# Kernel tuning notes

Hardware: AMD Instinct MI355X
Metric: run time of the kernel (lower is better)

## Reference

```python
import jax, jax.numpy as jnp
import numpy as np

EMB = 512
HEADS = 16
WH, WW = 8, 8
N = WH * WW
B = 2048
CPB_HID = 512
EPS = 1e-12


def _buffers():
    # continuous relative coords table, shape (1, 2*WH-1, 2*WW-1, 2)
    ch = np.arange(-(WH - 1), WH, dtype=np.float32)
    cw = np.arange(-(WW - 1), WW, dtype=np.float32)
    t = np.stack(np.meshgrid(ch, cw, indexing='ij')).transpose(1, 2, 0)[None].copy()
    t[..., 0] /= (WH - 1)
    t[..., 1] /= (WW - 1)
    t *= 8.0
    t = np.sign(t) * np.log2(np.abs(t) + 1.0) / np.log2(8.0)
    # relative position index, shape (N, N), values in [0, (2*WH-1)*(2*WW-1))
    coords = np.stack(np.meshgrid(np.arange(WH), np.arange(WW), indexing='ij'))
    cf = coords.reshape(2, -1)
    rel = (cf[:, :, None] - cf[:, None, :]).transpose(1, 2, 0).copy()
    rel[..., 0] += WH - 1
    rel[..., 1] += WW - 1
    rel[..., 0] *= 2 * WW - 1
    idx = rel.sum(-1)
    return jnp.asarray(t, jnp.float32), jnp.asarray(idx, jnp.int32)


def setup_inputs() -> dict:
    key = jax.random.key(0)
    ks = jax.random.split(key, 8)
    rel_table, rel_index = _buffers()
    s = 0.02
    return {
        'x': jax.random.normal(ks[0], (B, N, EMB), jnp.float32),
        'qkv_w': jax.random.normal(ks[1], (3 * EMB, EMB), jnp.float32) * s,
        'q_bias': jnp.zeros((EMB,), jnp.float32),
        'v_bias': jnp.zeros((EMB,), jnp.float32),
        'flex_attn': jnp.full((HEADS, 1, 1), np.log(10.0), jnp.float32),
        'cpb_w1': jax.random.normal(ks[2], (CPB_HID, 2), jnp.float32) * s,
        'cpb_b1': jnp.zeros((CPB_HID,), jnp.float32),
        'cpb_w2': jax.random.normal(ks[3], (HEADS, CPB_HID), jnp.float32) * s,
        'proj_w': jax.random.normal(ks[4], (EMB, EMB), jnp.float32) * s,
        'proj_b': jnp.zeros((EMB,), jnp.float32),
        'rel_table': rel_table,
        'rel_index': rel_index,
    }


def reference(x, qkv_w, q_bias, v_bias, flex_attn, cpb_w1, cpb_b1, cpb_w2,
              proj_w, proj_b, rel_table, rel_index):
    Bx, Nx, C = x.shape
    H = HEADS
    D = C // H
    # qkv with bias only on q and v (k bias is zero), as in the torch code
    qkv_bias = jnp.concatenate([q_bias, jnp.zeros_like(v_bias), v_bias])
    qkv = x @ qkv_w.T + qkv_bias                      # (B, N, 3C)
    qkv = qkv.reshape(Bx, Nx, 3, H, D).transpose(2, 0, 3, 1, 4)
    q, k, v = qkv[0], qkv[1], qkv[2]                  # each (B, H, N, D)
    # cosine attention: L2-normalize q and k
    qn = q / jnp.maximum(jnp.linalg.norm(q, axis=-1, keepdims=True), EPS)
    kn = k / jnp.maximum(jnp.linalg.norm(k, axis=-1, keepdims=True), EPS)
    attn = jnp.einsum('bhnd,bhmd->bhnm', qn, kn)      # (B, H, N, N)
    # learned per-head temperature, clamped at 1/0.01
    scale = jnp.exp(jnp.minimum(flex_attn, jnp.log(jnp.float32(100.0))))  # (H,1,1)
    attn = attn * scale[None]
    # continuous relative position bias via MLP + gather
    bias_tab = jax.nn.relu(rel_table @ cpb_w1.T + cpb_b1) @ cpb_w2.T      # (1, 2WH-1, 2WW-1, H)
    bias_tab = bias_tab.reshape(-1, H)
    bias = bias_tab[rel_index.reshape(-1)].reshape(Nx, Nx, H)
    bias = 16.0 * jax.nn.sigmoid(bias.transpose(2, 0, 1))                 # (H, N, N)
    attn = jax.nn.softmax(attn + bias[None], axis=-1)
    out = jnp.einsum('bhnm,bhmd->bhnd', attn, v)      # (B, H, N, D)
    out = out.transpose(0, 2, 1, 3).reshape(Bx, Nx, C)
    return out @ proj_w.T + proj_b
```

## Files before the change

### kernel.cpp

```cpp
#include <hip/hip_runtime.h>

using bf16x8 = __attribute__((ext_vector_type(8))) short;
using f32x4  = __attribute__((ext_vector_type(4))) float;

static constexpr int EMB = 512, HEADS = 16, NTOK = 64, BWIN = 2048;
static constexpr int MROWS = BWIN * NTOK;
static constexpr int QKVN  = 3 * EMB;

__device__ __forceinline__ float bf2f(unsigned int u) {
  union { unsigned int i; float f; } c; c.i = u << 16; return c.f;
}
__device__ __forceinline__ unsigned short f2bf(float x) {
  union { float f; unsigned int i; } c; c.f = x;
  return (unsigned short)((c.i + 0x7fffu + ((c.i >> 16) & 1u)) >> 16);
}
__device__ __forceinline__ void gload_lds16(const void* g, void* l) {
  __builtin_amdgcn_global_load_lds((const __attribute__((address_space(1))) void*)g,
                                   (__attribute__((address_space(3))) void*)l, 16, 0, 0);
}

#define BARRIER() __builtin_amdgcn_s_barrier()
#define LGKM0()  do { asm volatile("s_waitcnt lgkmcnt(0)" ::: "memory"); \
                      __builtin_amdgcn_sched_barrier(0); } while (0)
#define VMCNT2() do { asm volatile("s_waitcnt vmcnt(2)" ::: "memory"); \
                      __builtin_amdgcn_sched_barrier(0); } while (0)

__global__ __launch_bounds__(256) void xcast(const float* __restrict__ x,
                                             unsigned short* __restrict__ xb) {
  size_t i = ((size_t)blockIdx.x * 256 + threadIdx.x) * 8;
  float4 a = *(const float4*)(x + i);
  float4 b = *(const float4*)(x + i + 4);
  ushort4 lo = make_ushort4(f2bf(a.x), f2bf(a.y), f2bf(a.z), f2bf(a.w));
  ushort4 hi = make_ushort4(f2bf(b.x), f2bf(b.y), f2bf(b.z), f2bf(b.w));
  *(ushort4*)(xb + i) = lo;
  *(ushort4*)(xb + i + 4) = hi;
}

__global__ void prep_weights(const float* __restrict__ qkv_w, const float* __restrict__ proj_w,
                             const float* __restrict__ q_bias, const float* __restrict__ v_bias,
                             unsigned short* __restrict__ wq, unsigned short* __restrict__ wp,
                             float* __restrict__ qkv_bias) {
  int i = blockIdx.x * 256 + threadIdx.x;
  wq[i] = f2bf(qkv_w[i]);
  if (i < EMB * EMB) wp[i] = f2bf(proj_w[i]);
  if (i < EMB) {
    qkv_bias[i]           = q_bias[i];
    qkv_bias[EMB + i]     = 0.f;
    qkv_bias[2 * EMB + i] = v_bias[i];
  }
}

__global__ __launch_bounds__(64) void cpb_mlp(const float* __restrict__ tbl,
                        const float* __restrict__ w1, const float* __restrict__ b1,
                        const float* __restrict__ w2, float* __restrict__ tab) {
  __shared__ float hid[512];
  const int p = blockIdx.x, t = threadIdx.x;
  const float t0 = tbl[p * 2], t1 = tbl[p * 2 + 1];
  #pragma unroll
  for (int s = 0; s < 8; ++s) {
    int j = t + s * 64;
    hid[j] = fmaxf(0.f, t0 * w1[j * 2] + t1 * w1[j * 2 + 1] + b1[j]);
  }
  __syncthreads();
  const int h = t >> 2, q = t & 3;
  float sum = 0.f;
  for (int j = q * 128; j < q * 128 + 128; ++j) sum += hid[j] * w2[h * 512 + j];
  sum += __shfl_xor(sum, 1);
  sum += __shfl_xor(sum, 2);
  if (q == 0) tab[p * 16 + h] = sum;
}

__global__ void cpb_expand(const float* __restrict__ tab, const int* __restrict__ rel_index,
                           float* __restrict__ bias16) {
  int e = blockIdx.x * 256 + threadIdx.x;
  int h = e >> 12, ij = e & 4095;
  float x = tab[rel_index[ij] * 16 + h];
  bias16[e] = 16.f / (1.f + __expf(-x));
}

template<bool OUT_F32, int NBX, int KT>
__global__ __launch_bounds__(512, 2) void gemm256(const unsigned short* __restrict__ Ap,
    const unsigned short* __restrict__ Bp, const float* __restrict__ bias,
    void* __restrict__ Cp, int M, int N) {
  __shared__ unsigned short As[2][256 * 64];
  __shared__ unsigned short Bs[2][256 * 64];
  constexpr int NT = KT / 64;
  constexpr int NITER = NT / 2;
  const int t = threadIdx.x;
  const int l = t & 63, w = t >> 6;
  const int lr = l & 15, lg = l >> 4;
  const int q8 = gridDim.x >> 3;
  const int wgid = (blockIdx.x & 7) * q8 + (blockIdx.x >> 3);
  const int n0 = (wgid % NBX) * 256, m0 = (wgid / NBX) * 256;
  const int wm = (w >> 2) * 128, wn = (w & 3) * 64;
  const int ha128 = (w >> 2) * 128;
  const int srow = t >> 3;
  const int scol = ((t & 7) ^ (srow & 7)) << 3;
  const unsigned short* Abase = Ap + (size_t)m0 * KT;
  const unsigned short* Bbase = Bp + (size_t)n0 * KT;

  f32x4 acc[8][4];
  #pragma unroll
  for (int i = 0; i < 8; ++i)
    #pragma unroll
    for (int j = 0; j < 4; ++j) acc[i][j] = (f32x4){0.f, 0.f, 0.f, 0.f};
  bf16x8 afr[4][2], bfr[4][2];

  auto stage_half = [&](int d, int kt, int half, bool isA) {
    const unsigned short* g = (isA ? Abase : Bbase)
        + (size_t)(half * 128 + srow) * KT + kt * 64 + scol;
    unsigned short* lds = (isA ? &As[d][0] : &Bs[d][0]) + half * 8192 + (t >> 6) * 512;
    gload_lds16(g, lds);
    gload_lds16(g + (size_t)64 * KT, lds + 4096);
  };
  auto ldA4 = [&](int d, int mb) {
    #pragma unroll
    for (int m = 0; m < 4; ++m) {
      int row = ha128 + (mb + m) * 16 + lr;
      #pragma unroll
      for (int ks = 0; ks < 2; ++ks)
        afr[m][ks] = *(const bf16x8*)(&As[d][row * 64 + ((((ks << 2) + lg) ^ (lr & 7)) << 3)]);
    }
  };
  auto ldB2 = [&](int d, int nb) {
    #pragma unroll
    for (int n = 0; n < 2; ++n) {
      int row = wn + (nb + n) * 16 + lr;
      #pragma unroll
      for (int ks = 0; ks < 2; ++ks)
        bfr[nb + n][ks] = *(const bf16x8*)(&Bs[d][row * 64 + ((((ks << 2) + lg) ^ (lr & 7)) << 3)]);
    }
  };
  auto mfmaQ = [&](int mb, int nb) {
    __builtin_amdgcn_s_setprio(1);
    #pragma unroll
    for (int ks = 0; ks < 2; ++ks)
      #pragma unroll
      for (int m = 0; m < 4; ++m)
        #pragma unroll
        for (int n = 0; n < 2; ++n)
          acc[mb + m][nb + n] = __builtin_amdgcn_mfma_f32_16x16x32_bf16(
              afr[m][ks], bfr[nb + n][ks], acc[mb + m][nb + n], 0, 0, 0);
    __builtin_amdgcn_s_setprio(0);
  };

  stage_half(0, 0, 0, true);  stage_half(0, 0, 1, true);
  stage_half(0, 0, 0, false); stage_half(0, 0, 1, false);
  stage_half(1, (NT > 1 ? 1 : 0), 0, true);
  VMCNT2();
  BARRIER();

  for (int i = 0; i < NITER; ++i) {
    const int kt1 = 2 * i + 1;
    const int kt2 = (2 * i + 2 < NT) ? 2 * i + 2 : NT - 1;
    const int kt3 = (2 * i + 3 < NT) ? 2 * i + 3 : NT - 1;
    ldA4(0, 0); ldB2(0, 0);
    stage_half(1, kt1, 1, true);
    BARRIER(); LGKM0(); mfmaQ(0, 0); BARRIER();
    ldB2(0, 2);
    stage_half(1, kt1, 0, false);
    BARRIER(); LGKM0(); mfmaQ(0, 2); BARRIER();
    ldA4(0, 4);
    stage_half(1, kt1, 1, false);
    BARRIER(); LGKM0(); mfmaQ(4, 2); BARRIER();
    stage_half(0, kt2, 0, true);
    VMCNT2(); BARRIER(); mfmaQ(4, 0); BARRIER();
    ldA4(1, 0); ldB2(1, 0);
    stage_half(0, kt2, 1, true);
    BARRIER(); LGKM0(); mfmaQ(0, 0); BARRIER();
    ldB2(1, 2);
    stage_half(0, kt2, 0, false);
    BARRIER(); LGKM0(); mfmaQ(0, 2); BARRIER();
    ldA4(1, 4);
    stage_half(0, kt2, 1, false);
    BARRIER(); LGKM0(); mfmaQ(4, 2); BARRIER();
    stage_half(1, kt3, 0, true);
    VMCNT2(); BARRIER(); mfmaQ(4, 0); BARRIER();
  }

  #pragma unroll
  for (int mf = 0; mf < 8; ++mf)
    #pragma unroll
    for (int nf = 0; nf < 4; ++nf)
      #pragma unroll
      for (int r = 0; r < 4; ++r) {
        int mm = m0 + wm + mf * 16 + lg * 4 + r;
        int nn = n0 + wn + nf * 16 + lr;
        float v = acc[mf][nf][r] + bias[nn];
        if (OUT_F32) ((float*)Cp)[(size_t)mm * N + nn] = v;
        else ((unsigned short*)Cp)[(size_t)mm * N + nn] = f2bf(v);
      }
}

__device__ __forceinline__ bf16x8 load_norm_frag(const unsigned short* p, float s) {
  uint4 raw = *(const uint4*)p;
  float f[8];
  f[0] = bf2f(raw.x & 0xffffu); f[1] = bf2f(raw.x >> 16);
  f[2] = bf2f(raw.y & 0xffffu); f[3] = bf2f(raw.y >> 16);
  f[4] = bf2f(raw.z & 0xffffu); f[5] = bf2f(raw.z >> 16);
  f[6] = bf2f(raw.w & 0xffffu); f[7] = bf2f(raw.w >> 16);
  float ss = 0.f;
  #pragma unroll
  for (int j = 0; j < 8; ++j) ss += f[j] * f[j];
  ss += __shfl_xor(ss, 16);
  ss += __shfl_xor(ss, 32);
  float inv = s / fmaxf(sqrtf(ss), 1e-12f);
  bf16x8 v;
  #pragma unroll
  for (int j = 0; j < 8; ++j) v[j] = (short)f2bf(f[j] * inv);
  return v;
}

__global__ __launch_bounds__(64, 2) void attn_win(const unsigned short* __restrict__ qkv,
    const float* __restrict__ bias16, const float* __restrict__ flex,
    unsigned short* __restrict__ aout) {
  __shared__ __align__(16) char smem[16640];
  float* S           = (float*)smem;
  unsigned short* P  = (unsigned short*)smem;
  unsigned short* vT = (unsigned short*)(smem + 9216);
  const int l = threadIdx.x;
  const int lr = l & 15, lg = l >> 4;
  const int g = (blockIdx.x & 7) * (gridDim.x >> 3) + (blockIdx.x >> 3);
  const int b = g >> 4;
  const int h = g & 15;
  const unsigned short* base = qkv + (size_t)b * NTOK * QKVN;
  const float scale = __expf(fminf(flex[h], 4.6051701860f));

  const uint4* vp = (const uint4*)(base + (size_t)l * QKVN + 2 * EMB + h * 32);
  uint4 v0 = vp[0], v1 = vp[1], v2 = vp[2], v3 = vp[3];

  bf16x8 aq[4], bk[4];
  #pragma unroll
  for (int i = 0; i < 4; ++i)
    aq[i] = load_norm_frag(base + (size_t)(i * 16 + lr) * QKVN + h * 32 + lg * 8, scale);
  #pragma unroll
  for (int i = 0; i < 4; ++i)
    bk[i] = load_norm_frag(base + (size_t)(i * 16 + lr) * QKVN + EMB + h * 32 + lg * 8, 1.f);

  const f32x4 z = (f32x4){0.f, 0.f, 0.f, 0.f};
  f32x4 sacc[4][4];
  #pragma unroll
  for (int i = 0; i < 4; ++i)
    #pragma unroll
    for (int j = 0; j < 4; ++j)
      sacc[i][j] = __builtin_amdgcn_mfma_f32_16x16x32_bf16(aq[i], bk[j], z, 0, 0, 0);

  const float* bh = bias16 + (size_t)h * 4096;
  #pragma unroll
  for (int i = 0; i < 4; ++i)
    #pragma unroll
    for (int j = 0; j < 4; ++j)
      #pragma unroll
      for (int r = 0; r < 4; ++r) {
        int row = i * 16 + lg * 4 + r, col = j * 16 + lr;
        S[row * 65 + col] = sacc[i][j][r] + bh[row * 64 + col];
      }

  float rowv[64];
  float mx = -1e30f;
  #pragma unroll
  for (int j = 0; j < 64; ++j) { rowv[j] = S[l * 65 + j]; mx = fmaxf(mx, rowv[j]); }
  asm volatile("" ::: "memory");
  float sum = 0.f;
  #pragma unroll
  for (int s = 0; s < 8; ++s) {
    bf16x8 pk;
    #pragma unroll
    for (int m = 0; m < 8; ++m) {
      float e = __expf(rowv[s * 8 + m] - mx);
      sum += e;
      pk[m] = (short)f2bf(e);
    }
    *(bf16x8*)(P + l * 72 + s * 8) = pk;
  }
  const float inv = 1.f / sum;

  {
    unsigned int wd[16] = {v0.x, v0.y, v0.z, v0.w, v1.x, v1.y, v1.z, v1.w,
                           v2.x, v2.y, v2.z, v2.w, v3.x, v3.y, v3.z, v3.w};
    #pragma unroll
    for (int d = 0; d < 32; ++d) {
      unsigned short val = (d & 1) ? (unsigned short)(wd[d >> 1] >> 16)
                                   : (unsigned short)(wd[d >> 1] & 0xffffu);
      vT[d * 72 + l] = val;
    }
  }
  asm volatile("" ::: "memory");

  f32x4 oacc[4][2];
  #pragma unroll
  for (int i = 0; i < 4; ++i) { oacc[i][0] = z; oacc[i][1] = z; }
  #pragma unroll
  for (int ks = 0; ks < 2; ++ks) {
    bf16x8 ap[4], bv[2];
    #pragma unroll
    for (int i = 0; i < 4; ++i)
      ap[i] = *(const bf16x8*)(P + (i * 16 + lr) * 72 + ks * 32 + lg * 8);
    #pragma unroll
    for (int jd = 0; jd < 2; ++jd)
      bv[jd] = *(const bf16x8*)(vT + (jd * 16 + lr) * 72 + ks * 32 + lg * 8);
    #pragma unroll
    for (int i = 0; i < 4; ++i)
      #pragma unroll
      for (int jd = 0; jd < 2; ++jd)
        oacc[i][jd] = __builtin_amdgcn_mfma_f32_16x16x32_bf16(ap[i], bv[jd], oacc[i][jd], 0, 0, 0);
  }
  #pragma unroll
  for (int i = 0; i < 4; ++i)
    #pragma unroll
    for (int jd = 0; jd < 2; ++jd)
      #pragma unroll
      for (int r = 0; r < 4; ++r) {
        int tok = i * 16 + lg * 4 + r, d = jd * 16 + lr;
        float val = oacc[i][jd][r] * __shfl(inv, tok);
        aout[(size_t)(b * NTOK + tok) * EMB + h * 32 + d] = f2bf(val);
      }
}

extern "C" void kernel_launch(void* const* d_in, const int* in_sizes, int n_in,
                              void* d_out, int out_size, void* d_ws, size_t ws_size,
                              hipStream_t stream) {
  const float* x         = (const float*)d_in[0];
  const float* qkv_w     = (const float*)d_in[1];
  const float* q_bias    = (const float*)d_in[2];
  const float* v_bias    = (const float*)d_in[3];
  const float* flex      = (const float*)d_in[4];
  const float* cpb_w1    = (const float*)d_in[5];
  const float* cpb_b1    = (const float*)d_in[6];
  const float* cpb_w2    = (const float*)d_in[7];
  const float* proj_w    = (const float*)d_in[8];
  const float* proj_b    = (const float*)d_in[9];
  const float* rel_table = (const float*)d_in[10];
  const int*   rel_index = (const int*)d_in[11];

  char* ws = (char*)d_ws;
  unsigned short* qkv_bf = (unsigned short*)(ws + 0);
  unsigned short* xb     = (unsigned short*)(ws + 402653184ull);
  unsigned short* ao_bf  = (unsigned short*)(ws + 402653184ull);
  unsigned short* wq_bf  = (unsigned short*)(ws + 536870912ull);
  unsigned short* wp_bf  = (unsigned short*)(ws + 538443776ull);
  float* qkv_bias        = (float*)(ws + 538968064ull);
  float* tab             = (float*)(ws + 538974208ull);
  float* bias16          = (float*)(ws + 538988608ull);

  xcast<<<32768, 256, 0, stream>>>(x, xb);
  prep_weights<<<3072, 256, 0, stream>>>(qkv_w, proj_w, q_bias, v_bias, wq_bf, wp_bf, qkv_bias);
  cpb_mlp<<<225, 64, 0, stream>>>(rel_table, cpb_w1, cpb_b1, cpb_w2, tab);
  cpb_expand<<<256, 256, 0, stream>>>(tab, rel_index, bias16);
  gemm256<false, 6, EMB><<<3072, 512, 0, stream>>>(
      xb, wq_bf, qkv_bias, (void*)qkv_bf, MROWS, QKVN);
  attn_win<<<BWIN * HEADS, 64, 0, stream>>>(qkv_bf, bias16, flex, ao_bf);
  gemm256<true, 2, EMB><<<1024, 512, 0, stream>>>(
      ao_bf, wp_bf, proj_b, d_out, MROWS, EMB);
}
```

Before: 644.7 us.

## Shrink GEMM tile to 128x256 with K-step 32 and four blocks per CU

Replaces the 256x256 GEMM tile with a 128x256 tile and a 32-wide K step. The LDS footprint shrinks and a new XOR swizzle is used, which allows four blocks per CU instead of two. The pipeline schedule is reworked to fewer stages per iteration and the grid size doubles. This trades less data reuse per tile and more global traffic for higher occupancy and latency hiding; each wave now holds fewer accumulators.

```diff
diff --git a/kernel.cpp b/kernel.cpp
--- a/kernel.cpp
+++ b/kernel.cpp
@@ -22,7 +22,7 @@
 #define BARRIER() __builtin_amdgcn_s_barrier()
 #define LGKM0()  do { asm volatile("s_waitcnt lgkmcnt(0)" ::: "memory"); \
                       __builtin_amdgcn_sched_barrier(0); } while (0)
-#define VMCNT2() do { asm volatile("s_waitcnt vmcnt(2)" ::: "memory"); \
+#define VMCNT1() do { asm volatile("s_waitcnt vmcnt(1)" ::: "memory"); \
                       __builtin_amdgcn_sched_barrier(0); } while (0)
 
 __global__ __launch_bounds__(256) void xcast(const float* __restrict__ x,
@@ -79,107 +79,90 @@
 }
 
 template<bool OUT_F32, int NBX, int KT>
-__global__ __launch_bounds__(512, 2) void gemm256(const unsigned short* __restrict__ Ap,
+__global__ __launch_bounds__(512, 4) void gemm128(const unsigned short* __restrict__ Ap,
     const unsigned short* __restrict__ Bp, const float* __restrict__ bias,
     void* __restrict__ Cp, int M, int N) {
-  __shared__ unsigned short As[2][256 * 64];
-  __shared__ unsigned short Bs[2][256 * 64];
-  constexpr int NT = KT / 64;
+  __shared__ unsigned short As[2][128 * 32];
+  __shared__ unsigned short Bs[2][256 * 32];
+  constexpr int NT = KT / 32;
   constexpr int NITER = NT / 2;
   const int t = threadIdx.x;
   const int l = t & 63, w = t >> 6;
   const int lr = l & 15, lg = l >> 4;
   const int q8 = gridDim.x >> 3;
   const int wgid = (blockIdx.x & 7) * q8 + (blockIdx.x >> 3);
-  const int n0 = (wgid % NBX) * 256, m0 = (wgid / NBX) * 256;
-  const int wm = (w >> 2) * 128, wn = (w & 3) * 64;
-  const int ha128 = (w >> 2) * 128;
-  const int srow = t >> 3;
-  const int scol = ((t & 7) ^ (srow & 7)) << 3;
+  const int n0 = (wgid % NBX) * 256, m0 = (wgid / NBX) * 128;
+  const int wm = (w >> 2) * 64, wn = (w & 3) * 64;
+  const int srow = t >> 2;
+  const int sphys = t & 3;
   const unsigned short* Abase = Ap + (size_t)m0 * KT;
   const unsigned short* Bbase = Bp + (size_t)n0 * KT;
 
-  f32x4 acc[8][4];
-  #pragma unroll
-  for (int i = 0; i < 8; ++i)
+  f32x4 acc[4][4];
+  #pragma unroll
+  for (int i = 0; i < 4; ++i)
     #pragma unroll
     for (int j = 0; j < 4; ++j) acc[i][j] = (f32x4){0.f, 0.f, 0.f, 0.f};
-  bf16x8 afr[4][2], bfr[4][2];
-
-  auto stage_half = [&](int d, int kt, int half, bool isA) {
-    const unsigned short* g = (isA ? Abase : Bbase)
-        + (size_t)(half * 128 + srow) * KT + kt * 64 + scol;
-    unsigned short* lds = (isA ? &As[d][0] : &Bs[d][0]) + half * 8192 + (t >> 6) * 512;
-    gload_lds16(g, lds);
-    gload_lds16(g + (size_t)64 * KT, lds + 4096);
-  };
-  auto ldA4 = [&](int d, int mb) {
+  bf16x8 afr[4], bfr[4];
+
+  auto stageA = [&](int d, int kt) {
+    int logc = (sphys ^ ((srow >> 1) & 3)) << 3;
+    gload_lds16(Abase + (size_t)srow * KT + kt * 32 + logc, &As[d][w * 512]);
+  };
+  auto stageB = [&](int d, int kt, int pass) {
+    int row = pass * 128 + srow;
+    int logc = (sphys ^ ((row >> 1) & 3)) << 3;
+    gload_lds16(Bbase + (size_t)row * KT + kt * 32 + logc,
+                &Bs[d][pass * 4096 + w * 512]);
+  };
+  auto ldA4 = [&](int d) {
     #pragma unroll
     for (int m = 0; m < 4; ++m) {
-      int row = ha128 + (mb + m) * 16 + lr;
-      #pragma unroll
-      for (int ks = 0; ks < 2; ++ks)
-        afr[m][ks] = *(const bf16x8*)(&As[d][row * 64 + ((((ks << 2) + lg) ^ (lr & 7)) << 3)]);
+      int row = wm + m * 16 + lr;
+      afr[m] = *(const bf16x8*)(&As[d][row * 32 + ((lg ^ ((row >> 1) & 3)) << 3)]);
     }
   };
-  auto ldB2 = [&](int d, int nb) {
-    #pragma unroll
-    for (int n = 0; n < 2; ++n) {
-      int row = wn + (nb + n) * 16 + lr;
-      #pragma unroll
-      for (int ks = 0; ks < 2; ++ks)
-        bfr[nb + n][ks] = *(const bf16x8*)(&Bs[d][row * 64 + ((((ks << 2) + lg) ^ (lr & 7)) << 3)]);
+  auto ldB4 = [&](int d) {
+    #pragma unroll
+    for (int n = 0; n < 4; ++n) {
+      int row = wn + n * 16 + lr;
+      bfr[n] = *(const bf16x8*)(&Bs[d][row * 32 + ((lg ^ ((row >> 1) & 3)) << 3)]);
     }
   };
-  auto mfmaQ = [&](int mb, int nb) {
+  auto mfma8 = [&](int nb) {
     __builtin_amdgcn_s_setprio(1);
     #pragma unroll
-    for (int ks = 0; ks < 2; ++ks)
-      #pragma unroll
-      for (int m = 0; m < 4; ++m)
-        #pragma unroll
-        for (int n = 0; n < 2; ++n)
-          acc[mb + m][nb + n] = __builtin_amdgcn_mfma_f32_16x16x32_bf16(
-              afr[m][ks], bfr[nb + n][ks], acc[mb + m][nb + n], 0, 0, 0);
+    for (int m = 0; m < 4; ++m)
+      #pragma unroll
+      for (int n = 0; n < 2; ++n)
+        acc[m][nb + n] = __builtin_amdgcn_mfma_f32_16x16x32_bf16(
+            afr[m], bfr[nb + n], acc[m][nb + n], 0, 0, 0);
     __builtin_amdgcn_s_setprio(0);
   };
 
-  stage_half(0, 0, 0, true);  stage_half(0, 0, 1, true);
-  stage_half(0, 0, 0, false); stage_half(0, 0, 1, false);
-  stage_half(1, (NT > 1 ? 1 : 0), 0, true);
-  VMCNT2();
+  stageA(0, 0); stageB(0, 0, 0); stageB(0, 0, 1);
+  stageA(1, (NT > 1 ? 1 : 0));
+  VMCNT1();
   BARRIER();
 
   for (int i = 0; i < NITER; ++i) {
     const int kt1 = 2 * i + 1;
     const int kt2 = (2 * i + 2 < NT) ? 2 * i + 2 : NT - 1;
     const int kt3 = (2 * i + 3 < NT) ? 2 * i + 3 : NT - 1;
-    ldA4(0, 0); ldB2(0, 0);
-    stage_half(1, kt1, 1, true);
-    BARRIER(); LGKM0(); mfmaQ(0, 0); BARRIER();
-    ldB2(0, 2);
-    stage_half(1, kt1, 0, false);
-    BARRIER(); LGKM0(); mfmaQ(0, 2); BARRIER();
-    ldA4(0, 4);
-    stage_half(1, kt1, 1, false);
-    BARRIER(); LGKM0(); mfmaQ(4, 2); BARRIER();
-    stage_half(0, kt2, 0, true);
-    VMCNT2(); BARRIER(); mfmaQ(4, 0); BARRIER();
-    ldA4(1, 0); ldB2(1, 0);
-    stage_half(0, kt2, 1, true);
-    BARRIER(); LGKM0(); mfmaQ(0, 0); BARRIER();
-    ldB2(1, 2);
-    stage_half(0, kt2, 0, false);
-    BARRIER(); LGKM0(); mfmaQ(0, 2); BARRIER();
-    ldA4(1, 4);
-    stage_half(0, kt2, 1, false);
-    BARRIER(); LGKM0(); mfmaQ(4, 2); BARRIER();
-    stage_half(1, kt3, 0, true);
-    VMCNT2(); BARRIER(); mfmaQ(4, 0); BARRIER();
-  }
-
-  #pragma unroll
-  for (int mf = 0; mf < 8; ++mf)
+    ldA4(0); ldB4(0);
+    stageB(1, kt1, 0); stageB(1, kt1, 1);
+    BARRIER(); LGKM0(); mfma8(0); BARRIER();
+    stageA(0, kt2);
+    VMCNT1(); BARRIER(); mfma8(2); BARRIER();
+    ldA4(1); ldB4(1);
+    stageB(0, kt2, 0); stageB(0, kt2, 1);
+    BARRIER(); LGKM0(); mfma8(0); BARRIER();
+    stageA(1, kt3);
+    VMCNT1(); BARRIER(); mfma8(2); BARRIER();
+  }
+
+  #pragma unroll
+  for (int mf = 0; mf < 4; ++mf)
     #pragma unroll
     for (int nf = 0; nf < 4; ++nf)
       #pragma unroll
@@ -347,9 +330,9 @@
   prep_weights<<<3072, 256, 0, stream>>>(qkv_w, proj_w, q_bias, v_bias, wq_bf, wp_bf, qkv_bias);
   cpb_mlp<<<225, 64, 0, stream>>>(rel_table, cpb_w1, cpb_b1, cpb_w2, tab);
   cpb_expand<<<256, 256, 0, stream>>>(tab, rel_index, bias16);
-  gemm256<false, 6, EMB><<<3072, 512, 0, stream>>>(
+  gemm128<false, 6, EMB><<<6144, 512, 0, stream>>>(
       xb, wq_bf, qkv_bias, (void*)qkv_bf, MROWS, QKVN);
   attn_win<<<BWIN * HEADS, 64, 0, stream>>>(qkv_bf, bias16, flex, ao_bf);
-  gemm256<true, 2, EMB><<<1024, 512, 0, stream>>>(
+  gemm128<true, 2, EMB><<<2048, 512, 0, stream>>>(
       ao_bf, wp_bf, proj_b, d_out, MROWS, EMB);
 }
```

Result: no change. 656.4 us (+1.8%).

## Rewrite window attention with 32x32 MFMA and register-resident softmax

Applied to the files above, without the earlier changes.

The attention kernel now uses 32x32x16 MFMAs and computes S transposed (K times Q), so each lane holds one query column. Softmax then runs in registers with a single cross-half shuffle, instead of staging S and P through LDS. P is repacked for the PV MFMA with ds_bpermute and packed bf16 conversion. V is transposed into a smaller XOR-swizzled LDS tile, and the bias table is stored transposed to match the new layout. Less LDS also lets occupancy rise to 3 blocks per SIMD, at the cost of more register pressure and strided bias loads.

```diff
diff --git a/kernel.cpp b/kernel.cpp
--- a/kernel.cpp
+++ b/kernel.cpp
@@ -2,6 +2,7 @@
 
 using bf16x8 = __attribute__((ext_vector_type(8))) short;
 using f32x4  = __attribute__((ext_vector_type(4))) float;
+using f32x16 = __attribute__((ext_vector_type(16))) float;
 
 static constexpr int EMB = 512, HEADS = 16, NTOK = 64, BWIN = 2048;
 static constexpr int MROWS = BWIN * NTOK;
@@ -17,6 +18,11 @@
 __device__ __forceinline__ void gload_lds16(const void* g, void* l) {
   __builtin_amdgcn_global_load_lds((const __attribute__((address_space(1))) void*)g,
                                    (__attribute__((address_space(3))) void*)l, 16, 0, 0);
+}
+__device__ __forceinline__ unsigned int cvt_pk_bf16(float lo, float hi) {
+  unsigned int d;
+  asm("v_cvt_pk_bf16_f32 %0, %1, %2" : "=v"(d) : "v"(lo), "v"(hi));
+  return d;
 }
 
 #define BARRIER() __builtin_amdgcn_s_barrier()
@@ -71,11 +77,12 @@
 }
 
 __global__ void cpb_expand(const float* __restrict__ tab, const int* __restrict__ rel_index,
-                           float* __restrict__ bias16) {
+                           float* __restrict__ biasT) {
   int e = blockIdx.x * 256 + threadIdx.x;
   int h = e >> 12, ij = e & 4095;
-  float x = tab[rel_index[ij] * 16 + h];
-  bias16[e] = 16.f / (1.f + __expf(-x));
+  int kk = ij >> 6, q = ij & 63;
+  float x = tab[rel_index[q * 64 + kk] * 16 + h];
+  biasT[e] = 16.f / (1.f + __expf(-x));
 }
 
 template<bool OUT_F32, int NBX, int KT>
@@ -192,129 +199,126 @@
       }
 }
 
-__device__ __forceinline__ bf16x8 load_norm_frag(const unsigned short* p, float s) {
-  uint4 raw = *(const uint4*)p;
-  float f[8];
-  f[0] = bf2f(raw.x & 0xffffu); f[1] = bf2f(raw.x >> 16);
-  f[2] = bf2f(raw.y & 0xffffu); f[3] = bf2f(raw.y >> 16);
-  f[4] = bf2f(raw.z & 0xffffu); f[5] = bf2f(raw.z >> 16);
-  f[6] = bf2f(raw.w & 0xffffu); f[7] = bf2f(raw.w >> 16);
-  float ss = 0.f;
-  #pragma unroll
-  for (int j = 0; j < 8; ++j) ss += f[j] * f[j];
-  ss += __shfl_xor(ss, 16);
-  ss += __shfl_xor(ss, 32);
-  float inv = s / fmaxf(sqrtf(ss), 1e-12f);
-  bf16x8 v;
-  #pragma unroll
-  for (int j = 0; j < 8; ++j) v[j] = (short)f2bf(f[j] * inv);
-  return v;
-}
-
-__global__ __launch_bounds__(64, 2) void attn_win(const unsigned short* __restrict__ qkv,
-    const float* __restrict__ bias16, const float* __restrict__ flex,
+__global__ __launch_bounds__(64, 3) void attn_win(const unsigned short* __restrict__ qkv,
+    const float* __restrict__ biasT, const float* __restrict__ flex,
     unsigned short* __restrict__ aout) {
-  __shared__ __align__(16) char smem[16640];
-  float* S           = (float*)smem;
-  unsigned short* P  = (unsigned short*)smem;
-  unsigned short* vT = (unsigned short*)(smem + 9216);
+  __shared__ __align__(16) unsigned short vT[32 * 64];
   const int l = threadIdx.x;
-  const int lr = l & 15, lg = l >> 4;
+  const int lq = l & 31, hi = l >> 5;
   const int g = (blockIdx.x & 7) * (gridDim.x >> 3) + (blockIdx.x >> 3);
   const int b = g >> 4;
   const int h = g & 15;
   const unsigned short* base = qkv + (size_t)b * NTOK * QKVN;
   const float scale = __expf(fminf(flex[h], 4.6051701860f));
 
-  const uint4* vp = (const uint4*)(base + (size_t)l * QKVN + 2 * EMB + h * 32);
-  uint4 v0 = vp[0], v1 = vp[1], v2 = vp[2], v3 = vp[3];
-
-  bf16x8 aq[4], bk[4];
-  #pragma unroll
-  for (int i = 0; i < 4; ++i)
-    aq[i] = load_norm_frag(base + (size_t)(i * 16 + lr) * QKVN + h * 32 + lg * 8, scale);
-  #pragma unroll
-  for (int i = 0; i < 4; ++i)
-    bk[i] = load_norm_frag(base + (size_t)(i * 16 + lr) * QKVN + EMB + h * 32 + lg * 8, 1.f);
-
-  const f32x4 z = (f32x4){0.f, 0.f, 0.f, 0.f};
-  f32x4 sacc[4][4];
-  #pragma unroll
-  for (int i = 0; i < 4; ++i)
-    #pragma unroll
-    for (int j = 0; j < 4; ++j)
-      sacc[i][j] = __builtin_amdgcn_mfma_f32_16x16x32_bf16(aq[i], bk[j], z, 0, 0, 0);
-
-  const float* bh = bias16 + (size_t)h * 4096;
-  #pragma unroll
-  for (int i = 0; i < 4; ++i)
-    #pragma unroll
-    for (int j = 0; j < 4; ++j)
-      #pragma unroll
-      for (int r = 0; r < 4; ++r) {
-        int row = i * 16 + lg * 4 + r, col = j * 16 + lr;
-        S[row * 65 + col] = sacc[i][j][r] + bh[row * 64 + col];
-      }
-
-  float rowv[64];
-  float mx = -1e30f;
-  #pragma unroll
-  for (int j = 0; j < 64; ++j) { rowv[j] = S[l * 65 + j]; mx = fmaxf(mx, rowv[j]); }
-  asm volatile("" ::: "memory");
-  float sum = 0.f;
-  #pragma unroll
-  for (int s = 0; s < 8; ++s) {
-    bf16x8 pk;
-    #pragma unroll
-    for (int m = 0; m < 8; ++m) {
-      float e = __expf(rowv[s * 8 + m] - mx);
-      sum += e;
-      pk[m] = (short)f2bf(e);
-    }
-    *(bf16x8*)(P + l * 72 + s * 8) = pk;
-  }
-  const float inv = 1.f / sum;
-
   {
+    const uint4* vp = (const uint4*)(base + (size_t)l * QKVN + 2 * EMB + h * 32);
+    uint4 v0 = vp[0], v1 = vp[1], v2 = vp[2], v3 = vp[3];
     unsigned int wd[16] = {v0.x, v0.y, v0.z, v0.w, v1.x, v1.y, v1.z, v1.w,
                            v2.x, v2.y, v2.z, v2.w, v3.x, v3.y, v3.z, v3.w};
     #pragma unroll
     for (int d = 0; d < 32; ++d) {
       unsigned short val = (d & 1) ? (unsigned short)(wd[d >> 1] >> 16)
                                    : (unsigned short)(wd[d >> 1] & 0xffffu);
-      vT[d * 72 + l] = val;
-    }
-  }
+      vT[d * 64 + (((l >> 3) ^ (d & 7)) << 3) + (l & 7)] = val;
+    }
+  }
+
+  bf16x8 kfr[2][2], qfr[2][2];
+  #pragma unroll
+  for (int f = 0; f < 2; ++f) {
+    #pragma unroll
+    for (int which = 0; which < 2; ++which) {
+      const unsigned short* rp = base + (size_t)(f * 32 + lq) * QKVN
+                               + (which ? 0 : EMB) + h * 32 + hi * 8;
+      uint4 r0 = *(const uint4*)rp;
+      uint4 r1 = *(const uint4*)(rp + 16);
+      unsigned int wd[8] = {r0.x, r0.y, r0.z, r0.w, r1.x, r1.y, r1.z, r1.w};
+      float fv[16];
+      #pragma unroll
+      for (int e = 0; e < 8; ++e) {
+        fv[2 * e]     = bf2f(wd[e] & 0xffffu);
+        fv[2 * e + 1] = bf2f(wd[e] >> 16);
+      }
+      float ss = 0.f;
+      #pragma unroll
+      for (int e = 0; e < 16; ++e) ss += fv[e] * fv[e];
+      ss += __shfl_xor(ss, 32);
+      float inv = (which ? scale : 1.f) / fmaxf(sqrtf(ss), 1e-12f);
+      bf16x8 f0, f1;
+      #pragma unroll
+      for (int e = 0; e < 8; ++e) {
+        f0[e] = (short)f2bf(fv[e] * inv);
+        f1[e] = (short)f2bf(fv[8 + e] * inv);
+      }
+      if (which) { qfr[f][0] = f0; qfr[f][1] = f1; }
+      else       { kfr[f][0] = f0; kfr[f][1] = f1; }
+    }
+  }
+
   asm volatile("" ::: "memory");
 
-  f32x4 oacc[4][2];
-  #pragma unroll
-  for (int i = 0; i < 4; ++i) { oacc[i][0] = z; oacc[i][1] = z; }
-  #pragma unroll
-  for (int ks = 0; ks < 2; ++ks) {
-    bf16x8 ap[4], bv[2];
-    #pragma unroll
-    for (int i = 0; i < 4; ++i)
-      ap[i] = *(const bf16x8*)(P + (i * 16 + lr) * 72 + ks * 32 + lg * 8);
-    #pragma unroll
-    for (int jd = 0; jd < 2; ++jd)
-      bv[jd] = *(const bf16x8*)(vT + (jd * 16 + lr) * 72 + ks * 32 + lg * 8);
-    #pragma unroll
-    for (int i = 0; i < 4; ++i)
-      #pragma unroll
-      for (int jd = 0; jd < 2; ++jd)
-        oacc[i][jd] = __builtin_amdgcn_mfma_f32_16x16x32_bf16(ap[i], bv[jd], oacc[i][jd], 0, 0, 0);
-  }
-  #pragma unroll
-  for (int i = 0; i < 4; ++i)
-    #pragma unroll
-    for (int jd = 0; jd < 2; ++jd)
-      #pragma unroll
-      for (int r = 0; r < 4; ++r) {
-        int tok = i * 16 + lg * 4 + r, d = jd * 16 + lr;
-        float val = oacc[i][jd][r] * __shfl(inv, tok);
-        aout[(size_t)(b * NTOK + tok) * EMB + h * 32 + d] = f2bf(val);
+  bf16x8 bv[4];
+  #pragma unroll
+  for (int c = 0; c < 4; ++c)
+    bv[c] = *(const bf16x8*)(&vT[lq * 64 + ((((2 * c + hi) ^ (lq & 7))) << 3)]);
+
+  const f32x16 z16 = (f32x16)(0.f);
+
+  #pragma unroll
+  for (int qf = 0; qf < 2; ++qf) {
+    f32x16 s0 = __builtin_amdgcn_mfma_f32_32x32x16_bf16(kfr[0][0], qfr[qf][0], z16, 0, 0, 0);
+    s0 = __builtin_amdgcn_mfma_f32_32x32x16_bf16(kfr[0][1], qfr[qf][1], s0, 0, 0, 0);
+    f32x16 s1 = __builtin_amdgcn_mfma_f32_32x32x16_bf16(kfr[1][0], qfr[qf][0], z16, 0, 0, 0);
+    s1 = __builtin_amdgcn_mfma_f32_32x32x16_bf16(kfr[1][1], qfr[qf][1], s1, 0, 0, 0);
+
+    float p[32];
+    const float* bt = biasT + (size_t)h * 4096 + qf * 32 + lq;
+    #pragma unroll
+    for (int r = 0; r < 16; ++r) {
+      int kkb = (r & 3) + 8 * (r >> 2) + 4 * hi;
+      p[r]      = s0[r] + bt[kkb * 64];
+      p[16 + r] = s1[r] + bt[(32 + kkb) * 64];
+    }
+    float mx = p[0];
+    #pragma unroll
+    for (int e = 1; e < 32; ++e) mx = fmaxf(mx, p[e]);
+    mx = fmaxf(mx, __shfl_xor(mx, 32));
+    float sum = 0.f;
+    #pragma unroll
+    for (int e = 0; e < 32; ++e) { p[e] = __expf(p[e] - mx); sum += p[e]; }
+    sum += __shfl_xor(sum, 32);
+    const float inv = 1.f / sum;
+    #pragma unroll
+    for (int e = 0; e < 32; ++e) p[e] *= inv;
+
+    unsigned int wp_[2][8], sw[2][8];
+    #pragma unroll
+    for (int kf = 0; kf < 2; ++kf)
+      #pragma unroll
+      for (int m = 0; m < 8; ++m) {
+        wp_[kf][m] = cvt_pk_bf16(p[kf * 16 + 2 * m], p[kf * 16 + 2 * m + 1]);
+        sw[kf][m]  = (unsigned int)__builtin_amdgcn_ds_bpermute(
+                        ((l ^ 32) & 63) << 2, (int)wp_[kf][m]);
       }
+    f32x16 oacc = z16;
+    #pragma unroll
+    for (int c = 0; c < 4; ++c) {
+      const int kf = c >> 1, mlo = (c & 1) * 4;
+      unsigned int d0 = hi ? sw[kf][mlo + 2] : wp_[kf][mlo + 0];
+      unsigned int d1 = hi ? sw[kf][mlo + 3] : wp_[kf][mlo + 1];
+      unsigned int d2 = hi ? wp_[kf][mlo + 2] : sw[kf][mlo + 0];
+      unsigned int d3 = hi ? wp_[kf][mlo + 3] : sw[kf][mlo + 1];
+      union { uint4 u; bf16x8 v; } pa;
+      pa.u = make_uint4(d0, d1, d2, d3);
+      oacc = __builtin_amdgcn_mfma_f32_32x32x16_bf16(pa.v, bv[c], oacc, 0, 0, 0);
+    }
+    #pragma unroll
+    for (int r = 0; r < 16; ++r) {
+      int q = qf * 32 + (r & 3) + 8 * (r >> 2) + 4 * hi;
+      aout[(size_t)(b * NTOK + q) * EMB + h * 32 + lq] = f2bf(oacc[r]);
+    }
+  }
 }
 
 extern "C" void kernel_launch(void* const* d_in, const int* in_sizes, int n_in,
@@ -341,15 +345,15 @@
   unsigned short* wp_bf  = (unsigned short*)(ws + 538443776ull);
   float* qkv_bias        = (float*)(ws + 538968064ull);
   float* tab             = (float*)(ws + 538974208ull);
-  float* bias16          = (float*)(ws + 538988608ull);
+  float* biasT           = (float*)(ws + 538988608ull);
 
   xcast<<<32768, 256, 0, stream>>>(x, xb);
   prep_weights<<<3072, 256, 0, stream>>>(qkv_w, proj_w, q_bias, v_bias, wq_bf, wp_bf, qkv_bias);
   cpb_mlp<<<225, 64, 0, stream>>>(rel_table, cpb_w1, cpb_b1, cpb_w2, tab);
-  cpb_expand<<<256, 256, 0, stream>>>(tab, rel_index, bias16);
+  cpb_expand<<<256, 256, 0, stream>>>(tab, rel_index, biasT);
   gemm256<false, 6, EMB><<<3072, 512, 0, stream>>>(
       xb, wq_bf, qkv_bias, (void*)qkv_bf, MROWS, QKVN);
-  attn_win<<<BWIN * HEADS, 64, 0, stream>>>(qkv_bf, bias16, flex, ao_bf);
+  attn_win<<<BWIN * HEADS, 64, 0, stream>>>(qkv_bf, biasT, flex, ao_bf);
   gemm256<true, 2, EMB><<<1024, 512, 0, stream>>>(
       ao_bf, wp_bf, proj_b, d_out, MROWS, EMB);
 }
```

After: 637.3 us, median of 2. About the same (-1.1%).
